# Kernel optimization log

Measured on AMD Instinct MI355X. Metric: run time of the kernel, lower is better.

## Reference

```python
import jax, jax.numpy as jnp
import numpy as np

Q_LORA = 1536
KV_LORA = 512
ROPE_DIM = 64
NOPE_DIM = 128
NUM_HEADS = 16
QK_HEAD_DIM = NOPE_DIM + ROPE_DIM  # 192
HEAD_SIZE = KV_LORA + ROPE_DIM     # 576
MAX_POS = 4096
ROPE_BASE = 10000.0
T = 32768


def _rope_cos_sin(positions):
    # inv_freq: [ROPE_DIM//2]
    inv_freq = 1.0 / (ROPE_BASE ** (jnp.arange(0, ROPE_DIM, 2, dtype=jnp.float32) / ROPE_DIM))
    freqs = positions.astype(jnp.float32)[:, None] * inv_freq[None, :]  # [T, D/2]
    return jnp.cos(freqs), jnp.sin(freqs)


def _apply_rope_neox(x, cos, sin):
    # x: [T, H, D]; cos/sin: [T, D/2] broadcast over heads
    x1, x2 = jnp.split(x, 2, axis=-1)
    c = cos[:, None, :]
    s = sin[:, None, :]
    return jnp.concatenate([x1 * c - x2 * s, x2 * c + x1 * s], axis=-1)


def setup_inputs() -> dict:
    key = jax.random.key(0)
    k1, k2, k3 = jax.random.split(key, 3)
    qkv_lora = jax.random.normal(k1, (T, Q_LORA + KV_LORA + ROPE_DIM), dtype=jnp.float32)
    positions = jax.random.randint(k2, (T,), 0, MAX_POS, dtype=jnp.int64)
    Wq = jax.random.normal(k3, (Q_LORA, NUM_HEADS * QK_HEAD_DIM), dtype=jnp.float32) * 0.02
    kv_cache = jnp.zeros((T, HEAD_SIZE), dtype=jnp.float32)
    slot_mapping = jnp.arange(T, dtype=jnp.int64)
    return {"qkv_lora": qkv_lora, "positions": positions, "Wq": Wq,
            "kv_cache": kv_cache, "slot_mapping": slot_mapping}


def reference(qkv_lora, positions, Wq, kv_cache, slot_mapping):
    # split low-rank projections
    q_c = qkv_lora[:, :Q_LORA]                               # [T, 1536]
    kv_c = qkv_lora[:, Q_LORA:Q_LORA + KV_LORA]              # [T, 512]
    k_pe = qkv_lora[:, Q_LORA + KV_LORA:]                    # [T, 64]

    # q_b_proj GEMM then reshape to heads
    q = (q_c @ Wq).reshape(T, NUM_HEADS, QK_HEAD_DIM)        # [T, H, 192]

    # RoPE on q rope slice and k_pe (neox style)
    cos, sin = _rope_cos_sin(positions)
    q_pe = _apply_rope_neox(q[..., NOPE_DIM:], cos, sin)     # [T, H, 64]
    k_pe_rot = _apply_rope_neox(k_pe[:, None, :], cos, sin)  # [T, 1, 64]
    q = jnp.concatenate([q[..., :NOPE_DIM], q_pe], axis=-1)

    # paged KV cache scatter write: concat(kv_c, k_pe) at slot_mapping
    entry = jnp.concatenate([kv_c, k_pe_rot[:, 0, :]], axis=-1)  # [T, 576]
    kv_cache = kv_cache.at[slot_mapping].set(entry)

    return q, kv_c, k_pe_rot, kv_cache
```

## Files before the change

### kernel.cpp

```cpp
#include <hip/hip_runtime.h>
#include <hip/hip_bf16.h>
#include <stdint.h>

typedef unsigned short ushort_t;
typedef __attribute__((ext_vector_type(4))) float f32x4;
typedef __attribute__((ext_vector_type(8))) short short8;

#define T_TOK 32768
#define QL    1536
#define KVL   512
#define RD    64
#define NQ    3072
#define ROWW  2112
#define HS    576

#define BM 256
#define BN 256
#define BK 64
#define KT (QL / BK)
#define MT (T_TOK / BM)
#define NT (NQ / BN)

#define NLOG (-0.28782313662425572f)

static __device__ __forceinline__ short f2bf(float x) {
  __hip_bfloat16 h = __float2bfloat16(x);
  return *reinterpret_cast<short*>(&h);
}

#define GLOAD16(gp, lp)                                        \
  __builtin_amdgcn_global_load_lds(                            \
      (const __attribute__((address_space(1))) void*)(gp),     \
      (__attribute__((address_space(3))) void*)(lp), 16, 0, 0)

__global__ __launch_bounds__(256) void aconv_kernel(const float* __restrict__ qkv,
                                                    ushort_t* __restrict__ Abf) {
  int g = blockIdx.x * 256 + threadIdx.x;
  int row = g / 192;
  int col = (g - row * 192) * 8;
  const float* s = qkv + (size_t)row * ROWW + col;
  f32x4 a = *(const f32x4*)s;
  f32x4 b = *(const f32x4*)(s + 4);
  short8 v;
  v[0] = f2bf(a[0]); v[1] = f2bf(a[1]); v[2] = f2bf(a[2]); v[3] = f2bf(a[3]);
  v[4] = f2bf(b[0]); v[5] = f2bf(b[1]); v[6] = f2bf(b[2]); v[7] = f2bf(b[3]);
  *(short8*)(Abf + (size_t)row * QL + col) = v;
}

__global__ void wq_t_kernel(const float* __restrict__ Wq, ushort_t* __restrict__ Wt) {
  __shared__ float tile[32][33];
  int tx = threadIdx.x, ty = threadIdx.y;
  int n0 = blockIdx.x * 32, k0 = blockIdx.y * 32;
#pragma unroll
  for (int j = 0; j < 32; j += 8)
    tile[ty + j][tx] = Wq[(size_t)(k0 + ty + j) * NQ + n0 + tx];
  __syncthreads();
#pragma unroll
  for (int j = 0; j < 32; j += 8)
    Wt[(size_t)(n0 + ty + j) * QL + k0 + tx] = f2bf(tile[tx][ty + j]);
}

__global__ __launch_bounds__(512, 2) void gemm_rope_kernel(
    const ushort_t* __restrict__ Abf, const int* __restrict__ pos,
    const ushort_t* __restrict__ wt, float* __restrict__ out_q) {
  __shared__ ushort_t lds[2][2][2][256 * 32];

  int bid = blockIdx.x;
  int vb = (bid & 7) * (MT * NT / 8) + (bid >> 3);
  int m0 = (vb / NT) * BM;
  int n0 = (vb % NT) * BN;

  int tid = threadIdx.x;
  int wv = tid >> 6, ln = tid & 63;
  int l16 = ln & 15, lq4 = ln >> 4;
  int wm = wv >> 2, wn = wv & 3;

  int srow = wv * 32 + (ln >> 2);
  int schunk = ((ln & 3) ^ ((ln >> 3) & 3)) * 8;
  const ushort_t* aS = Abf + (size_t)(m0 + srow) * QL + schunk;
  const ushort_t* bS = wt  + (size_t)(n0 + srow) * QL + schunk;
  int sdst = wv * 32 * 32;

#define STG(PAR, AB, KH, TT, SRC) do {                                         \
    GLOAD16((SRC) + (size_t)(TT) * BK + (KH) * 32,           &lds[PAR][AB][KH][sdst]);       \
    GLOAD16((SRC) + (size_t)(TT) * BK + (KH) * 32 + 16 * QL, &lds[PAR][AB][KH][sdst + 512]); \
  } while (0)

  int rkey = (l16 >> 1) & 3;
  int aoff = (wm * 128 + l16) * 32 + (lq4 ^ rkey) * 8;
  int boff = (wn * 64  + l16) * 32 + (lq4 ^ rkey) * 8;

  f32x4 acc[8][4];
#pragma unroll
  for (int i = 0; i < 8; ++i)
#pragma unroll
    for (int j = 0; j < 4; ++j) acc[i][j] = (f32x4)0.0f;

  STG(0, 0, 0, 0, aS);
  STG(0, 1, 0, 0, bS);
  STG(0, 0, 1, 0, aS);
  STG(0, 1, 1, 0, bS);
  STG(1, 0, 0, 1, aS);
  STG(1, 1, 0, 1, bS);
  asm volatile("s_waitcnt vmcnt(8)" ::: "memory");
  __builtin_amdgcn_s_barrier();

#define MFMA_PHASE(ACCBASE)                                                    \
  __builtin_amdgcn_s_barrier();                                                \
  asm volatile("s_waitcnt lgkmcnt(0)" ::: "memory");                           \
  __builtin_amdgcn_sched_barrier(0);                                           \
  __builtin_amdgcn_s_setprio(1);                                               \
  _Pragma("unroll")                                                            \
  for (int q = 0; q < 4; ++q)                                                  \
    _Pragma("unroll")                                                          \
    for (int n = 0; n < 4; ++n)                                                \
      acc[(ACCBASE) + q][n] = __builtin_amdgcn_mfma_f32_16x16x32_bf16(         \
          af[q], bf[n], acc[(ACCBASE) + q][n], 0, 0, 0);                       \
  __builtin_amdgcn_s_setprio(0);                                               \
  __builtin_amdgcn_s_barrier();

  for (int t = 0; t < KT; ++t) {
    int par = t & 1;
    const ushort_t* Ak0 = &lds[par][0][0][0];
    const ushort_t* Bk0 = &lds[par][1][0][0];
    const ushort_t* Ak1 = &lds[par][0][1][0];
    const ushort_t* Bk1 = &lds[par][1][1][0];
    short8 af[4], bf[4];

#pragma unroll
    for (int q = 0; q < 4; ++q) af[q] = *(const short8*)(Ak0 + aoff + q * 512);
#pragma unroll
    for (int n = 0; n < 4; ++n) bf[n] = *(const short8*)(Bk0 + boff + n * 512);
    if (t + 1 < KT) STG(par ^ 1, 0, 1, t + 1, aS);
    MFMA_PHASE(0)

#pragma unroll
    for (int q = 0; q < 4; ++q) af[q] = *(const short8*)(Ak0 + aoff + (4 + q) * 512);
    if (t < KT - 1) { asm volatile("s_waitcnt vmcnt(6)" ::: "memory"); }
    else            { asm volatile("s_waitcnt vmcnt(0)" ::: "memory"); }
    if (t + 1 < KT) STG(par ^ 1, 1, 1, t + 1, bS);
    MFMA_PHASE(4)

#pragma unroll
    for (int q = 0; q < 4; ++q) af[q] = *(const short8*)(Ak1 + aoff + q * 512);
#pragma unroll
    for (int n = 0; n < 4; ++n) bf[n] = *(const short8*)(Bk1 + boff + n * 512);
    if (t + 2 < KT) STG(par, 0, 0, t + 2, aS);
    MFMA_PHASE(0)

#pragma unroll
    for (int q = 0; q < 4; ++q) af[q] = *(const short8*)(Ak1 + aoff + (4 + q) * 512);
    if (t < KT - 2)       { asm volatile("s_waitcnt vmcnt(6)" ::: "memory"); }
    else if (t == KT - 2) { asm volatile("s_waitcnt vmcnt(4)" ::: "memory"); }
    if (t + 2 < KT) STG(par, 1, 0, t + 2, bS);
    MFMA_PHASE(4)
  }

  int gn = n0 + wn * 64;
  bool ropew = ((gn % 192) == 128);
  if (!ropew) {
#pragma unroll
    for (int mi = 0; mi < 8; ++mi)
#pragma unroll
      for (int r = 0; r < 4; ++r) {
        int t = m0 + wm * 128 + mi * 16 + lq4 * 4 + r;
        float* rowp = out_q + (size_t)t * NQ + gn + l16;
        rowp[0]  = acc[mi][0][r];
        rowp[16] = acc[mi][1][r];
        rowp[32] = acc[mi][2][r];
        rowp[48] = acc[mi][3][r];
      }
  } else {
    float invf0 = __expf((float)l16 * NLOG);
    float invf1 = __expf((float)(l16 + 16) * NLOG);
#pragma unroll
    for (int mi = 0; mi < 8; ++mi)
#pragma unroll
      for (int r = 0; r < 4; ++r) {
        int t = m0 + wm * 128 + mi * 16 + lq4 * 4 + r;
        float p = (float)pos[t];
        float s0, c0, s1, c1;
        __sincosf(p * invf0, &s0, &c0);
        __sincosf(p * invf1, &s1, &c1);
        float x1a = acc[mi][0][r], x1b = acc[mi][1][r];
        float x2a = acc[mi][2][r], x2b = acc[mi][3][r];
        float* rowp = out_q + (size_t)t * NQ + gn + l16;
        rowp[0]  = x1a * c0 - x2a * s0;
        rowp[16] = x1b * c1 - x2b * s1;
        rowp[32] = x2a * c0 + x1a * s0;
        rowp[48] = x2b * c1 + x1b * s1;
      }
  }
}

__global__ void kv_kernel(const float* __restrict__ qkv, const int* __restrict__ pos,
                          const int* __restrict__ slots,
                          float* __restrict__ out_kvc, float* __restrict__ out_kpe,
                          float* __restrict__ out_cache) {
  int tok = blockIdx.x * 4 + (threadIdx.x >> 6);
  int lane = threadIdx.x & 63;
  const float* src = qkv + (size_t)tok * ROWW + QL;
  float* dkv = out_kvc + (size_t)tok * KVL;
  int slot = slots[tok];
  float* dc = out_cache + (size_t)slot * HS;
#pragma unroll
  for (int i = 0; i < 2; ++i) {
    f32x4 v = *(const f32x4*)(src + (size_t)(lane + 64 * i) * 4);
    *(f32x4*)(dkv + (size_t)(lane + 64 * i) * 4) = v;
    *(f32x4*)(dc + (size_t)(lane + 64 * i) * 4) = v;
  }
  if (lane < 32) {
    float x1 = src[KVL + lane], x2 = src[KVL + 32 + lane];
    float p = (float)pos[tok];
    float invf = __expf((float)lane * NLOG);
    float s, c;
    __sincosf(p * invf, &s, &c);
    float r1 = x1 * c - x2 * s;
    float r2 = x2 * c + x1 * s;
    out_kpe[(size_t)tok * RD + lane] = r1;
    out_kpe[(size_t)tok * RD + 32 + lane] = r2;
    dc[KVL + lane] = r1;
    dc[KVL + 32 + lane] = r2;
  }
}

extern "C" void kernel_launch(void* const* d_in, const int* in_sizes, int n_in,
                              void* d_out, int out_size, void* d_ws, size_t ws_size,
                              hipStream_t stream) {
  const float* qkv       = (const float*)d_in[0];
  const int*   positions = (const int*)d_in[1];
  const float* Wq        = (const float*)d_in[2];
  const int*   slots     = (const int*)d_in[4];

  float* out_q     = (float*)d_out;
  float* out_kvc   = out_q   + (size_t)T_TOK * NQ;
  float* out_kpe   = out_kvc + (size_t)T_TOK * KVL;
  float* out_cache = out_kpe + (size_t)T_TOK * RD;

  size_t abf_bytes = (size_t)T_TOK * QL * sizeof(ushort_t);
  size_t wt_bytes  = (size_t)NQ * QL * sizeof(ushort_t);
  char* scratch = (ws_size >= abf_bytes + wt_bytes) ? (char*)d_ws : (char*)out_kvc;
  ushort_t* Abf = (ushort_t*)scratch;
  ushort_t* Wt  = (ushort_t*)(scratch + abf_bytes);

  aconv_kernel<<<dim3(T_TOK * 192 / 256), dim3(256), 0, stream>>>(qkv, Abf);
  wq_t_kernel<<<dim3(NQ / 32, QL / 32), dim3(32, 8), 0, stream>>>(Wq, Wt);
  gemm_rope_kernel<<<dim3(MT * NT), dim3(512), 0, stream>>>(Abf, positions, Wt, out_q);
  kv_kernel<<<dim3(T_TOK / 4), dim3(256), 0, stream>>>(qkv, positions, slots,
                                                       out_kvc, out_kpe, out_cache);
}
```

Baseline: 440.4 us.

## Restructure GEMM main loop to two barriers per k-step with larger MFMA clusters

The bf16 GEMM main loop is reorganized from four MFMA phases, each wrapped in barriers and an lgkmcnt wait, into two halves per k-step. Each half loads all A and B fragments for a 32-wide k slice up front and then issues 32 MFMAs back to back. The global-to-LDS staging for the next tiles is grouped per half, with one vmcnt wait per iteration. This is meant to cut barrier and wait overhead and give longer uninterrupted MFMA runs, at the cost of more live fragment registers and reliance on the new barrier placement being correct for LDS hazards.

```diff
diff --git a/kernel.cpp b/kernel.cpp
--- a/kernel.cpp
+++ b/kernel.cpp
@@ -102,58 +102,65 @@
   STG(0, 1, 1, 0, bS);
   STG(1, 0, 0, 1, aS);
   STG(1, 1, 0, 1, bS);
-  asm volatile("s_waitcnt vmcnt(8)" ::: "memory");
-  __builtin_amdgcn_s_barrier();
-
-#define MFMA_PHASE(ACCBASE)                                                    \
-  __builtin_amdgcn_s_barrier();                                                \
-  asm volatile("s_waitcnt lgkmcnt(0)" ::: "memory");                           \
-  __builtin_amdgcn_sched_barrier(0);                                           \
+
+#define CLUSTER(ACCBASE, AF)                                                   \
   __builtin_amdgcn_s_setprio(1);                                               \
   _Pragma("unroll")                                                            \
   for (int q = 0; q < 4; ++q)                                                  \
     _Pragma("unroll")                                                          \
     for (int n = 0; n < 4; ++n)                                                \
       acc[(ACCBASE) + q][n] = __builtin_amdgcn_mfma_f32_16x16x32_bf16(         \
-          af[q], bf[n], acc[(ACCBASE) + q][n], 0, 0, 0);                       \
-  __builtin_amdgcn_s_setprio(0);                                               \
-  __builtin_amdgcn_s_barrier();
-
+          AF[q], bf[n], acc[(ACCBASE) + q][n], 0, 0, 0);                       \
+  __builtin_amdgcn_s_setprio(0);
+
+#pragma unroll 2
   for (int t = 0; t < KT; ++t) {
     int par = t & 1;
     const ushort_t* Ak0 = &lds[par][0][0][0];
     const ushort_t* Bk0 = &lds[par][1][0][0];
     const ushort_t* Ak1 = &lds[par][0][1][0];
     const ushort_t* Bk1 = &lds[par][1][1][0];
-    short8 af[4], bf[4];
-
-#pragma unroll
-    for (int q = 0; q < 4; ++q) af[q] = *(const short8*)(Ak0 + aoff + q * 512);
-#pragma unroll
-    for (int n = 0; n < 4; ++n) bf[n] = *(const short8*)(Bk0 + boff + n * 512);
-    if (t + 1 < KT) STG(par ^ 1, 0, 1, t + 1, aS);
-    MFMA_PHASE(0)
-
-#pragma unroll
-    for (int q = 0; q < 4; ++q) af[q] = *(const short8*)(Ak0 + aoff + (4 + q) * 512);
-    if (t < KT - 1) { asm volatile("s_waitcnt vmcnt(6)" ::: "memory"); }
-    else            { asm volatile("s_waitcnt vmcnt(0)" ::: "memory"); }
-    if (t + 1 < KT) STG(par ^ 1, 1, 1, t + 1, bS);
-    MFMA_PHASE(4)
-
-#pragma unroll
-    for (int q = 0; q < 4; ++q) af[q] = *(const short8*)(Ak1 + aoff + q * 512);
-#pragma unroll
-    for (int n = 0; n < 4; ++n) bf[n] = *(const short8*)(Bk1 + boff + n * 512);
-    if (t + 2 < KT) STG(par, 0, 0, t + 2, aS);
-    MFMA_PHASE(0)
-
-#pragma unroll
-    for (int q = 0; q < 4; ++q) af[q] = *(const short8*)(Ak1 + aoff + (4 + q) * 512);
-    if (t < KT - 2)       { asm volatile("s_waitcnt vmcnt(6)" ::: "memory"); }
-    else if (t == KT - 2) { asm volatile("s_waitcnt vmcnt(4)" ::: "memory"); }
-    if (t + 2 < KT) STG(par, 1, 0, t + 2, bS);
-    MFMA_PHASE(4)
+    short8 af0[4], af1[4], bf[4];
+
+    __builtin_amdgcn_sched_barrier(0);
+    if (t == KT - 1) { asm volatile("s_waitcnt vmcnt(0)" ::: "memory"); }
+    else             { asm volatile("s_waitcnt vmcnt(4)" ::: "memory"); }
+    __builtin_amdgcn_s_barrier();
+    __builtin_amdgcn_sched_barrier(0);
+
+#pragma unroll
+    for (int q = 0; q < 4; ++q) af0[q] = *(const short8*)(Ak0 + aoff + q * 512);
+#pragma unroll
+    for (int n = 0; n < 4; ++n) bf[n]  = *(const short8*)(Bk0 + boff + n * 512);
+#pragma unroll
+    for (int q = 0; q < 4; ++q) af1[q] = *(const short8*)(Ak0 + aoff + (4 + q) * 512);
+    if (t + 1 < KT) { STG(par ^ 1, 0, 1, t + 1, aS); STG(par ^ 1, 1, 1, t + 1, bS); }
+
+    CLUSTER(0, af0)
+    CLUSTER(4, af1)
+
+    short8 ag0[4], ag1[4], bg[4];
+#pragma unroll
+    for (int q = 0; q < 4; ++q) ag0[q] = *(const short8*)(Ak1 + aoff + q * 512);
+#pragma unroll
+    for (int n = 0; n < 4; ++n) bg[n]  = *(const short8*)(Bk1 + boff + n * 512);
+#pragma unroll
+    for (int q = 0; q < 4; ++q) ag1[q] = *(const short8*)(Ak1 + aoff + (4 + q) * 512);
+
+    __builtin_amdgcn_sched_barrier(0);
+    __builtin_amdgcn_s_barrier();
+    __builtin_amdgcn_sched_barrier(0);
+
+    if (t + 2 < KT) { STG(par, 0, 0, t + 2, aS); STG(par, 1, 0, t + 2, bS); }
+
+    {
+      short8* bfp = bg;
+#define bf bg
+      CLUSTER(0, ag0)
+      CLUSTER(4, ag1)
+#undef bf
+      (void)bfp;
+    }
   }
 
   int gn = n0 + wn * 64;
```

Result: no change. 439.3 us (-0.3%).
